# Kernel tuning notes

Measured on AMD Instinct MI355X. Metric: run time of the kernel, lower is better.

## Reference

```python
import jax, jax.numpy as jnp
import numpy as np
import math

ITERATIONS = 2
STRIDE = 1
ALPHA = 0.0
MEAN_DATA = 1.0
FINAL_LAMBDA = 0.01  # final_beta
EPS = 1e-7
MIN_VAR_ADD = 0.0005


def setup_inputs() -> dict:
    key = jax.random.key(0)
    k1, k2 = jax.random.split(key)
    b, h, w, k, i, o, a = 2, 12, 12, 3, 32, 32, 4
    votes = jax.random.normal(k1, (b, h, w, k, k, i, o, a, a), dtype=jnp.float32)
    acts = jax.random.uniform(k2, (b, h, w, k, k, i, 1, 1, 1), dtype=jnp.float32)
    beta_a = jnp.full((1, 1, 1, 1, 1, 1, o, 1, 1), 0.5, dtype=jnp.float32)
    beta_u = jnp.full((1, 1, 1, 1, 1, 1, o, 1, 1), 0.5, dtype=jnp.float32)
    return {"votes": votes, "acts": acts, "beta_a": beta_a, "beta_u": beta_u}


def reference(votes, acts, beta_a, beta_u):
    b, h, w, k = votes.shape[0], votes.shape[1], votes.shape[2], votes.shape[3]
    i, o, a = votes.shape[5], votes.shape[6], votes.shape[7]
    s = STRIDE
    Hr = h * s + k - s  # reconstructed height
    Wr = w * s + k - s
    # target spatial coords for each (h,y) / (w,x) of the kernel window
    Y = jnp.arange(h)[:, None] * s + jnp.arange(k)[None, :]  # (h,k)
    X = jnp.arange(w)[:, None] * s + jnp.arange(k)[None, :]  # (w,k)
    lin = (Y[:, None, :, None] * Wr + X[None, :, None, :]).reshape(-1)  # (h*w*k*k,)

    # R_ij init: softmax over zeros along out-capsule axis -> uniform 1/o
    R = jnp.full((b, h, w, k, k, i, o, 1, 1), 1.0 / o, dtype=votes.dtype)
    out_poses = jnp.zeros((b, h, w, 1, 1, 1, o, a, a), dtype=votes.dtype)

    def m_step(R, out_poses, it):
        Ra = R * acts                                   # (b,h,w,k,k,i,o,1,1)
        sumR = jnp.sum(Ra, axis=(3, 4, 5), keepdims=True)
        mu = jnp.sum(Ra * votes, axis=(3, 4, 5), keepdims=True) / (sumR + EPS)
        mu = (1.0 - ALPHA) * mu + ALPHA * out_poses     # (b,h,w,1,1,1,o,a,a)
        sig = jnp.sum(Ra * jnp.square(votes - mu), axis=(3, 4, 5), keepdims=True) / (sumR + EPS) + MIN_VAR_ADD
        cost = (beta_u - 0.5 * jnp.log(sig + EPS)) * sumR / MEAN_DATA
        inv_temp = FINAL_LAMBDA * (1.0 - 0.95 ** (it + 1))
        a_j = jax.nn.sigmoid(inv_temp * (beta_a - jnp.sum(cost, axis=(-1, -2), keepdims=True)))
        return mu, sig, a_j

    def e_step(mu, sig, a_j):
        log_p = -jnp.sum(jnp.log(2.0 * math.pi * sig) + jnp.square(votes - mu) / (2.0 * sig),
                         axis=(-1, -2), keepdims=True)        # (b,h,w,k,k,i,o,1,1)
        lognum = jnp.log(a_j) + log_p
        ap = jnp.exp(lognum - jnp.max(lognum))                # global-max shift as in original
        # scatter-add (fold / col2im) onto the reconstructed grid, then sum over o
        ap6 = ap.reshape(b, h, w, k, k, i, o)
        ap_t = ap6.transpose(1, 2, 3, 4, 0, 5, 6).reshape(h * w * k * k, b, i, o)
        dense = jax.ops.segment_sum(ap_t, lin, num_segments=Hr * Wr)  # (Hr*Wr,b,i,o)
        dense = dense.sum(-1).reshape(Hr, Wr, b, i)
        # extract_patches: gather the window sums back to (b,h,w,k,k,i)
        denom = dense[Y[:, None, :, None], X[None, :, None, :]]  # (h,w,k,k,b,i)
        denom = jnp.transpose(denom, (4, 0, 1, 2, 3, 5))[..., None, None, None]
        return ap / (denom + EPS)

    for it in range(ITERATIONS - 1):
        mu, sig, a_j = m_step(R, out_poses, it)
        out_poses = mu
        R = e_step(mu, sig, a_j)
    mu, sig, a_j = m_step(R, out_poses, ITERATIONS)

    poses = jnp.squeeze(mu, axis=(3, 4, 5))     # (b,h,w,o,a,a)
    acts_out = jnp.squeeze(a_j, axis=(3, 4, 5))  # (b,h,w,o,1,1)
    return poses, acts_out
```

## Files before the change

### kernel.cpp

```cpp
#include <hip/hip_runtime.h>
#include <math.h>

#define NB 2
#define NH 12
#define NW 12
#define NK 3
#define NI 32
#define NO 32
#define NA 16
#define NBHW (NB*NH*NW)
#define NC (NK*NK*NI)
#define CSTR (NO*NA)
#define VPB (NC*CSTR)
#define HR 14
#define WR 14
#define EPSF 1e-7f
#define MINVAR 5e-4f
#define TEMP0 0.0005f
#define TEMPF 0.00142625f

#define CH 8
#define CPC (NC/CH)
#define ITERS (CPC/2)
#define NBLK (NBHW*CH)

#define PA_S1 0
#define PA_S2 (PA_S1 + NBLK*512)
#define PA_SR (PA_S2 + NBLK*512)
#define PD_S1 (PA_SR + NBLK)
#define PD_S2 (PD_S1 + NBLK*512)
#define PD_SR (PD_S2 + NBLK*512)
#define MU_OFF (PD_SR + NBLK*32)
#define W_OFF  (MU_OFF + NBHW*512)
#define L_OFF  (W_OFF + NBHW*512)
#define BM_OFF (L_OFF + NBHW*32)
#define M_OFF  (BM_OFF + NBLK)
#define DENSE_OFF (M_OFF + 16)
#define DENSE_N (NB*HR*WR*NI)
#define LOGNUM_OFF (DENSE_OFF + DENSE_N)

__global__ __launch_bounds__(256) void kA(const float* __restrict__ votes,
        const float* __restrict__ acts, float* __restrict__ ws) {
    __shared__ float s_acts[CPC];
    __shared__ float4 r1[128], r2[128];
    __shared__ float sR1;
    const int bid = blockIdx.x;
    const int bhw = bid >> 3;
    const int cbase = (bid & 7) * CPC;
    const int t = threadIdx.x;
    if (t < CPC) s_acts[t] = acts[bhw*NC + cbase + t] * (1.0f/NO);
    __syncthreads();
    const int child_sub = t >> 7;
    const int rem = t & 127;
    const float4* vb4 = (const float4*)votes + (size_t)bhw*(VPB/4);
    float s1[4] = {0,0,0,0}, s2[4] = {0,0,0,0};
    float sumR = 0.f;
    #pragma unroll 6
    for (int it = 0; it < ITERS; ++it) {
        const int c_loc = it*2 + child_sub;
        float4 v = vb4[(size_t)(cbase + c_loc)*128 + rem];
        float ra = s_acts[c_loc];
        s1[0] += ra*v.x; s2[0] = fmaf(ra*v.x, v.x, s2[0]);
        s1[1] += ra*v.y; s2[1] = fmaf(ra*v.y, v.y, s2[1]);
        s1[2] += ra*v.z; s2[2] = fmaf(ra*v.z, v.z, s2[2]);
        s1[3] += ra*v.w; s2[3] = fmaf(ra*v.w, v.w, s2[3]);
        sumR += ra;
    }
    if (child_sub) {
        r1[rem] = make_float4(s1[0], s1[1], s1[2], s1[3]);
        r2[rem] = make_float4(s2[0], s2[1], s2[2], s2[3]);
        if (rem == 0) sR1 = sumR;
    }
    __syncthreads();
    if (!child_sub) {
        float4 o1 = r1[rem], o2 = r2[rem];
        ((float4*)(ws + PA_S1))[bid*128 + rem] =
            make_float4(s1[0]+o1.x, s1[1]+o1.y, s1[2]+o1.z, s1[3]+o1.w);
        ((float4*)(ws + PA_S2))[bid*128 + rem] =
            make_float4(s2[0]+o2.x, s2[1]+o2.y, s2[2]+o2.z, s2[3]+o2.w);
        if (rem == 0) ws[PA_SR + bid] = sumR + sR1;
    }
}

__global__ __launch_bounds__(256) void kA2(const float* __restrict__ beta_a,
        const float* __restrict__ beta_u, float* __restrict__ ws) {
    const int bid = blockIdx.x;
    const int bhw = bid >> 1;
    const int obase = (bid & 1) * 16;
    const int t = threadIdx.x;
    const int a = t & 15;
    const int o = obase + (t >> 4);
    const int idx = o*16 + a;
    float s1 = 0.f, s2 = 0.f, sumR = 0.f;
    #pragma unroll
    for (int ch = 0; ch < 8; ++ch) {
        s1   += ws[PA_S1 + (size_t)(bhw*8 + ch)*512 + idx];
        s2   += ws[PA_S2 + (size_t)(bhw*8 + ch)*512 + idx];
        sumR += ws[PA_SR + bhw*8 + ch];
    }
    float mu  = s1 / (sumR + EPSF);
    float sig = (s2 - mu*(2.f*s1 - mu*sumR)) / (sumR + EPSF) + MINVAR;
    ws[MU_OFF + bhw*512 + a*32 + o] = mu;
    ws[W_OFF  + bhw*512 + a*32 + o] = 0.5f / sig;
    float cost = (beta_u[o] - 0.5f*logf(sig + EPSF)) * sumR;
    float ps   = logf(6.2831853071795864f * sig);
    #pragma unroll
    for (int d = 1; d < 16; d <<= 1) {
        cost += __shfl_xor(cost, d);
        ps   += __shfl_xor(ps, d);
    }
    if (a == 0) {
        float aj = 1.0f/(1.0f + expf(-TEMP0*(beta_a[o] - cost)));
        ws[L_OFF + bhw*32 + o] = logf(aj) - ps;
    }
}

__global__ __launch_bounds__(256) void kB(const float* __restrict__ votes,
                                          float* __restrict__ ws) {
    const int bid = blockIdx.x;
    const int bhw = bid >> 3;
    const int cbase = (bid & 7) * CPC;
    const int t = threadIdx.x;
    const int child_sub = t >> 7;
    const int rem = t & 127;
    const int o = rem >> 2;
    const int quad = rem & 3;
    float mur[4], wr[4];
    #pragma unroll
    for (int j = 0; j < 4; ++j) {
        mur[j] = ws[MU_OFF + bhw*512 + (quad*4+j)*32 + o];
        wr[j]  = ws[W_OFF  + bhw*512 + (quad*4+j)*32 + o];
    }
    const float L = ws[L_OFF + bhw*32 + o];
    const float4* vb4 = (const float4*)votes + (size_t)bhw*(VPB/4);
    float* lp = ws + LOGNUM_OFF + (size_t)bhw*(NC*NO);
    float tmax = -3.0e38f;
    #pragma unroll 6
    for (int it = 0; it < ITERS; ++it) {
        const int c = cbase + it*2 + child_sub;
        float4 v = vb4[(size_t)c*128 + rem];
        float d0 = v.x - mur[0];
        float acc = d0*d0*wr[0];
        float d1 = v.y - mur[1]; acc = fmaf(d1*d1, wr[1], acc);
        float d2 = v.z - mur[2]; acc = fmaf(d2*d2, wr[2], acc);
        float d3 = v.w - mur[3]; acc = fmaf(d3*d3, wr[3], acc);
        acc += __shfl_xor(acc, 1);
        acc += __shfl_xor(acc, 2);
        float ln = L - acc;
        if (quad == 0) lp[c*32 + o] = ln;
        tmax = fmaxf(tmax, ln);
    }
    #pragma unroll
    for (int d = 1; d < 64; d <<= 1) tmax = fmaxf(tmax, __shfl_xor(tmax, d));
    __shared__ float smax[4];
    if ((t & 63) == 0) smax[t >> 6] = tmax;
    __syncthreads();
    if (t == 0)
        ws[BM_OFF + bid] = fmaxf(fmaxf(smax[0], smax[1]), fmaxf(smax[2], smax[3]));
}

__global__ __launch_bounds__(256) void kBmax(float* __restrict__ ws) {
    const int t = threadIdx.x;
    float m = -3.0e38f;
    for (int i = t; i < NBLK; i += 256) m = fmaxf(m, ws[BM_OFF + i]);
    #pragma unroll
    for (int d = 1; d < 64; d <<= 1) m = fmaxf(m, __shfl_xor(m, d));
    __shared__ float sm[4];
    if ((t & 63) == 0) sm[t >> 6] = m;
    __syncthreads();
    if (t == 0) ws[M_OFF] = fmaxf(fmaxf(sm[0], sm[1]), fmaxf(sm[2], sm[3]));
}

__global__ __launch_bounds__(256) void kC(float* __restrict__ ws) {
    const int bid = blockIdx.x;
    const int bhw = bid >> 2;
    const int cbase = (bid & 3) * 72;
    const int t = threadIdx.x;
    const int b = bhw / (NH*NW);
    const int rem = bhw % (NH*NW);
    const int y = rem / NW, x = rem % NW;
    const float M = ws[M_OFF];
    const float* lp = ws + LOGNUM_OFF + (size_t)bhw*(NC*NO);
    float* dense = ws + DENSE_OFF;
    const int o = t & 31;
    for (int it = 0; it < 9; ++it) {
        const int c = cbase + it*8 + (t >> 5);
        float s = expf(lp[c*32 + o] - M);
        #pragma unroll
        for (int d = 1; d < 32; d <<= 1) s += __shfl_xor(s, d);
        if (o == 0) {
            const int i = c & 31, kk = c >> 5;
            const int ky = kk / 3, kx = kk % 3;
            atomicAdd(&dense[((b*HR + y+ky)*WR + (x+kx))*NI + i], s);
        }
    }
}

__global__ __launch_bounds__(256) void kD(const float* __restrict__ votes,
        const float* __restrict__ acts, float* __restrict__ ws) {
    __shared__ float s_rd[CPC];
    __shared__ float s_ra[CPC*NO];
    __shared__ float4 r1[128], r2[128];
    __shared__ float sSR[64];
    const int bid = blockIdx.x;
    const int bhw = bid >> 3;
    const int cbase = (bid & 7) * CPC;
    const int t = threadIdx.x;
    const int b = bhw / (NH*NW);
    const int remhw = bhw % (NH*NW);
    const int y = remhw / NW, x = remhw % NW;
    if (t < CPC) {
        const int c = cbase + t;
        const int i = c & 31, kk = c >> 5;
        const int ky = kk / 3, kx = kk % 3;
        float dn = ws[DENSE_OFF + ((b*HR + y+ky)*WR + (x+kx))*NI + i];
        s_rd[t] = acts[bhw*NC + c] / (dn + EPSF);
    }
    __syncthreads();
    const float M = ws[M_OFF];
    const float* lp = ws + LOGNUM_OFF + (size_t)bhw*(NC*NO) + (size_t)cbase*32;
    for (int idx = t; idx < CPC*NO; idx += 256)
        s_ra[idx] = s_rd[idx >> 5] * expf(lp[idx] - M);
    __syncthreads();
    const int child_sub = t >> 7;
    const int rem = t & 127;
    const int o = rem >> 2;
    const int quad = rem & 3;
    const float4* vb4 = (const float4*)votes + (size_t)bhw*(VPB/4);
    float s1[4] = {0,0,0,0}, s2[4] = {0,0,0,0};
    float sumR = 0.f;
    #pragma unroll 6
    for (int it = 0; it < ITERS; ++it) {
        const int c_loc = it*2 + child_sub;
        float4 v = vb4[(size_t)(cbase + c_loc)*128 + rem];
        float ra = s_ra[c_loc*32 + o];
        s1[0] += ra*v.x; s2[0] = fmaf(ra*v.x, v.x, s2[0]);
        s1[1] += ra*v.y; s2[1] = fmaf(ra*v.y, v.y, s2[1]);
        s1[2] += ra*v.z; s2[2] = fmaf(ra*v.z, v.z, s2[2]);
        s1[3] += ra*v.w; s2[3] = fmaf(ra*v.w, v.w, s2[3]);
        sumR += ra;
    }
    if (quad == 0) sSR[child_sub*32 + o] = sumR;
    if (child_sub) {
        r1[rem] = make_float4(s1[0], s1[1], s1[2], s1[3]);
        r2[rem] = make_float4(s2[0], s2[1], s2[2], s2[3]);
    }
    __syncthreads();
    if (!child_sub) {
        float4 o1 = r1[rem], o2 = r2[rem];
        ((float4*)(ws + PD_S1))[bid*128 + rem] =
            make_float4(s1[0]+o1.x, s1[1]+o1.y, s1[2]+o1.z, s1[3]+o1.w);
        ((float4*)(ws + PD_S2))[bid*128 + rem] =
            make_float4(s2[0]+o2.x, s2[1]+o2.y, s2[2]+o2.z, s2[3]+o2.w);
    }
    if (t < 32) ws[PD_SR + bid*32 + t] = sSR[t] + sSR[32 + t];
}

__global__ __launch_bounds__(256) void kD2(const float* __restrict__ beta_a,
        const float* __restrict__ beta_u, const float* __restrict__ ws,
        float* __restrict__ out) {
    const int bid = blockIdx.x;
    const int bhw = bid >> 1;
    const int obase = (bid & 1) * 16;
    const int t = threadIdx.x;
    const int a = t & 15;
    const int o = obase + (t >> 4);
    float s1 = 0.f, s2 = 0.f, sumR = 0.f;
    #pragma unroll
    for (int ch = 0; ch < 8; ++ch) {
        s1   += ws[PD_S1 + (size_t)(bhw*8 + ch)*512 + obase*16 + t];
        s2   += ws[PD_S2 + (size_t)(bhw*8 + ch)*512 + obase*16 + t];
        sumR += ws[PD_SR + (bhw*8 + ch)*32 + o];
    }
    float mu  = s1 / (sumR + EPSF);
    float sig = (s2 - mu*(2.f*s1 - mu*sumR)) / (sumR + EPSF) + MINVAR;
    out[bhw*512 + obase*16 + t] = mu;
    float cost = (beta_u[o] - 0.5f*logf(sig + EPSF)) * sumR;
    #pragma unroll
    for (int d = 1; d < 16; d <<= 1) cost += __shfl_xor(cost, d);
    if (a == 0) {
        float aj = 1.0f/(1.0f + expf(-TEMPF*(beta_a[o] - cost)));
        out[NBHW*512 + bhw*32 + o] = aj;
    }
}

extern "C" void kernel_launch(void* const* d_in, const int* in_sizes, int n_in,
                              void* d_out, int out_size, void* d_ws, size_t ws_size,
                              hipStream_t stream) {
    const float* votes  = (const float*)d_in[0];
    const float* acts   = (const float*)d_in[1];
    const float* beta_a = (const float*)d_in[2];
    const float* beta_u = (const float*)d_in[3];
    float* ws  = (float*)d_ws;
    float* out = (float*)d_out;

    hipMemsetAsync(ws + DENSE_OFF, 0, DENSE_N*sizeof(float), stream);
    kA   <<<NBLK,   256, 0, stream>>>(votes, acts, ws);
    kA2  <<<NBHW*2, 256, 0, stream>>>(beta_a, beta_u, ws);
    kB   <<<NBLK,   256, 0, stream>>>(votes, ws);
    kBmax<<<1,      256, 0, stream>>>(ws);
    kC   <<<NBHW*4, 256, 0, stream>>>(ws);
    kD   <<<NBLK,   256, 0, stream>>>(votes, acts, ws);
    kD2  <<<NBHW*2, 256, 0, stream>>>(beta_a, beta_u, ws, out);
}
```

Measured before the change: 317.3 us.

## Fuse reduction kernels into neighbors, drop memset, and halve chunk split

Removes the memset, kA2 and kBmax launches. Dense zeroing now happens inside kA. The per-bhw mu/sigma/L finalisation is computed redundantly in each kB block into shared memory. Each block of kC and kD recomputes the global max from the per-block maxima. Chunks per bhw drop from 8 to 4, which halves the block count but doubles the per-block loop length. This cuts launch overhead and intermediate global round-trips, at the cost of redundant finalisation work and lower parallelism over the 1.3 MB-per-bhw vote stream.

```diff
diff --git a/kernel.cpp b/kernel.cpp
--- a/kernel.cpp
+++ b/kernel.cpp
@@ -19,7 +19,7 @@
 #define TEMP0 0.0005f
 #define TEMPF 0.00142625f
 
-#define CH 8
+#define CH 4
 #define CPC (NC/CH)
 #define ITERS (CPC/2)
 #define NBLK (NBHW*CH)
@@ -30,12 +30,8 @@
 #define PD_S1 (PA_SR + NBLK)
 #define PD_S2 (PD_S1 + NBLK*512)
 #define PD_SR (PD_S2 + NBLK*512)
-#define MU_OFF (PD_SR + NBLK*32)
-#define W_OFF  (MU_OFF + NBHW*512)
-#define L_OFF  (W_OFF + NBHW*512)
-#define BM_OFF (L_OFF + NBHW*32)
-#define M_OFF  (BM_OFF + NBLK)
-#define DENSE_OFF (M_OFF + 16)
+#define BM_OFF (PD_SR + NBLK*32)
+#define DENSE_OFF (BM_OFF + NBLK)
 #define DENSE_N (NB*HR*WR*NI)
 #define LOGNUM_OFF (DENSE_OFF + DENSE_N)
 
@@ -45,9 +41,13 @@
     __shared__ float4 r1[128], r2[128];
     __shared__ float sR1;
     const int bid = blockIdx.x;
-    const int bhw = bid >> 3;
-    const int cbase = (bid & 7) * CPC;
-    const int t = threadIdx.x;
+    const int bhw = bid >> 2;
+    const int cbase = (bid & 3) * CPC;
+    const int t = threadIdx.x;
+    {
+        const int idx = bid*256 + t;
+        if (idx < DENSE_N) ws[DENSE_OFF + idx] = 0.f;
+    }
     if (t < CPC) s_acts[t] = acts[bhw*NC + cbase + t] * (1.0f/NO);
     __syncthreads();
     const int child_sub = t >> 7;
@@ -82,45 +82,44 @@
     }
 }
 
-__global__ __launch_bounds__(256) void kA2(const float* __restrict__ beta_a,
-        const float* __restrict__ beta_u, float* __restrict__ ws) {
-    const int bid = blockIdx.x;
-    const int bhw = bid >> 1;
-    const int obase = (bid & 1) * 16;
-    const int t = threadIdx.x;
-    const int a = t & 15;
-    const int o = obase + (t >> 4);
-    const int idx = o*16 + a;
-    float s1 = 0.f, s2 = 0.f, sumR = 0.f;
-    #pragma unroll
-    for (int ch = 0; ch < 8; ++ch) {
-        s1   += ws[PA_S1 + (size_t)(bhw*8 + ch)*512 + idx];
-        s2   += ws[PA_S2 + (size_t)(bhw*8 + ch)*512 + idx];
-        sumR += ws[PA_SR + bhw*8 + ch];
-    }
-    float mu  = s1 / (sumR + EPSF);
-    float sig = (s2 - mu*(2.f*s1 - mu*sumR)) / (sumR + EPSF) + MINVAR;
-    ws[MU_OFF + bhw*512 + a*32 + o] = mu;
-    ws[W_OFF  + bhw*512 + a*32 + o] = 0.5f / sig;
-    float cost = (beta_u[o] - 0.5f*logf(sig + EPSF)) * sumR;
-    float ps   = logf(6.2831853071795864f * sig);
-    #pragma unroll
-    for (int d = 1; d < 16; d <<= 1) {
-        cost += __shfl_xor(cost, d);
-        ps   += __shfl_xor(ps, d);
-    }
-    if (a == 0) {
-        float aj = 1.0f/(1.0f + expf(-TEMP0*(beta_a[o] - cost)));
-        ws[L_OFF + bhw*32 + o] = logf(aj) - ps;
-    }
-}
-
 __global__ __launch_bounds__(256) void kB(const float* __restrict__ votes,
-                                          float* __restrict__ ws) {
-    const int bid = blockIdx.x;
-    const int bhw = bid >> 3;
-    const int cbase = (bid & 7) * CPC;
-    const int t = threadIdx.x;
+        const float* __restrict__ beta_a, const float* __restrict__ beta_u,
+        float* __restrict__ ws) {
+    __shared__ float s_mu[512], s_w[512], s_L[32], smax[4];
+    const int bid = blockIdx.x;
+    const int bhw = bid >> 2;
+    const int cbase = (bid & 3) * CPC;
+    const int t = threadIdx.x;
+    float sumR = 0.f;
+    #pragma unroll
+    for (int ch = 0; ch < CH; ++ch) sumR += ws[PA_SR + bhw*CH + ch];
+    #pragma unroll
+    for (int half = 0; half < 2; ++half) {
+        const int idx = t + half*256;
+        float s1 = 0.f, s2 = 0.f;
+        #pragma unroll
+        for (int ch = 0; ch < CH; ++ch) {
+            s1 += ws[PA_S1 + (size_t)(bhw*CH + ch)*512 + idx];
+            s2 += ws[PA_S2 + (size_t)(bhw*CH + ch)*512 + idx];
+        }
+        const int o = idx >> 4, a = idx & 15;
+        float mu  = s1 / (sumR + EPSF);
+        float sig = (s2 - mu*(2.f*s1 - mu*sumR)) / (sumR + EPSF) + MINVAR;
+        s_mu[a*32 + o] = mu;
+        s_w [a*32 + o] = 0.5f / sig;
+        float cost = (beta_u[o] - 0.5f*logf(sig + EPSF)) * sumR;
+        float ps   = logf(6.2831853071795864f * sig);
+        #pragma unroll
+        for (int d = 1; d < 16; d <<= 1) {
+            cost += __shfl_xor(cost, d);
+            ps   += __shfl_xor(ps, d);
+        }
+        if (a == 0) {
+            float aj = 1.0f/(1.0f + expf(-TEMP0*(beta_a[o] - cost)));
+            s_L[o] = logf(aj) - ps;
+        }
+    }
+    __syncthreads();
     const int child_sub = t >> 7;
     const int rem = t & 127;
     const int o = rem >> 2;
@@ -128,10 +127,10 @@
     float mur[4], wr[4];
     #pragma unroll
     for (int j = 0; j < 4; ++j) {
-        mur[j] = ws[MU_OFF + bhw*512 + (quad*4+j)*32 + o];
-        wr[j]  = ws[W_OFF  + bhw*512 + (quad*4+j)*32 + o];
-    }
-    const float L = ws[L_OFF + bhw*32 + o];
+        mur[j] = s_mu[(quad*4 + j)*32 + o];
+        wr[j]  = s_w [(quad*4 + j)*32 + o];
+    }
+    const float L = s_L[o];
     const float4* vb4 = (const float4*)votes + (size_t)bhw*(VPB/4);
     float* lp = ws + LOGNUM_OFF + (size_t)bhw*(NC*NO);
     float tmax = -3.0e38f;
@@ -152,38 +151,32 @@
     }
     #pragma unroll
     for (int d = 1; d < 64; d <<= 1) tmax = fmaxf(tmax, __shfl_xor(tmax, d));
-    __shared__ float smax[4];
     if ((t & 63) == 0) smax[t >> 6] = tmax;
     __syncthreads();
     if (t == 0)
         ws[BM_OFF + bid] = fmaxf(fmaxf(smax[0], smax[1]), fmaxf(smax[2], smax[3]));
 }
 
-__global__ __launch_bounds__(256) void kBmax(float* __restrict__ ws) {
+__global__ __launch_bounds__(256) void kC(float* __restrict__ ws) {
+    __shared__ float smax[4];
+    const int bid = blockIdx.x;
+    const int bhw = bid >> 2;
+    const int cbase = (bid & 3) * CPC;
     const int t = threadIdx.x;
     float m = -3.0e38f;
     for (int i = t; i < NBLK; i += 256) m = fmaxf(m, ws[BM_OFF + i]);
     #pragma unroll
     for (int d = 1; d < 64; d <<= 1) m = fmaxf(m, __shfl_xor(m, d));
-    __shared__ float sm[4];
-    if ((t & 63) == 0) sm[t >> 6] = m;
-    __syncthreads();
-    if (t == 0) ws[M_OFF] = fmaxf(fmaxf(sm[0], sm[1]), fmaxf(sm[2], sm[3]));
-}
-
-__global__ __launch_bounds__(256) void kC(float* __restrict__ ws) {
-    const int bid = blockIdx.x;
-    const int bhw = bid >> 2;
-    const int cbase = (bid & 3) * 72;
-    const int t = threadIdx.x;
+    if ((t & 63) == 0) smax[t >> 6] = m;
+    __syncthreads();
+    const float M = fmaxf(fmaxf(smax[0], smax[1]), fmaxf(smax[2], smax[3]));
     const int b = bhw / (NH*NW);
     const int rem = bhw % (NH*NW);
     const int y = rem / NW, x = rem % NW;
-    const float M = ws[M_OFF];
     const float* lp = ws + LOGNUM_OFF + (size_t)bhw*(NC*NO);
     float* dense = ws + DENSE_OFF;
     const int o = t & 31;
-    for (int it = 0; it < 9; ++it) {
+    for (int it = 0; it < CPC/8; ++it) {
         const int c = cbase + it*8 + (t >> 5);
         float s = expf(lp[c*32 + o] - M);
         #pragma unroll
@@ -200,15 +193,21 @@
         const float* __restrict__ acts, float* __restrict__ ws) {
     __shared__ float s_rd[CPC];
     __shared__ float s_ra[CPC*NO];
+    __shared__ float smax[4];
     __shared__ float4 r1[128], r2[128];
     __shared__ float sSR[64];
     const int bid = blockIdx.x;
-    const int bhw = bid >> 3;
-    const int cbase = (bid & 7) * CPC;
+    const int bhw = bid >> 2;
+    const int cbase = (bid & 3) * CPC;
     const int t = threadIdx.x;
     const int b = bhw / (NH*NW);
     const int remhw = bhw % (NH*NW);
     const int y = remhw / NW, x = remhw % NW;
+    float m = -3.0e38f;
+    for (int i = t; i < NBLK; i += 256) m = fmaxf(m, ws[BM_OFF + i]);
+    #pragma unroll
+    for (int d = 1; d < 64; d <<= 1) m = fmaxf(m, __shfl_xor(m, d));
+    if ((t & 63) == 0) smax[t >> 6] = m;
     if (t < CPC) {
         const int c = cbase + t;
         const int i = c & 31, kk = c >> 5;
@@ -217,7 +216,7 @@
         s_rd[t] = acts[bhw*NC + c] / (dn + EPSF);
     }
     __syncthreads();
-    const float M = ws[M_OFF];
+    const float M = fmaxf(fmaxf(smax[0], smax[1]), fmaxf(smax[2], smax[3]));
     const float* lp = ws + LOGNUM_OFF + (size_t)bhw*(NC*NO) + (size_t)cbase*32;
     for (int idx = t; idx < CPC*NO; idx += 256)
         s_ra[idx] = s_rd[idx >> 5] * expf(lp[idx] - M);
@@ -267,10 +266,10 @@
     const int o = obase + (t >> 4);
     float s1 = 0.f, s2 = 0.f, sumR = 0.f;
     #pragma unroll
-    for (int ch = 0; ch < 8; ++ch) {
-        s1   += ws[PD_S1 + (size_t)(bhw*8 + ch)*512 + obase*16 + t];
-        s2   += ws[PD_S2 + (size_t)(bhw*8 + ch)*512 + obase*16 + t];
-        sumR += ws[PD_SR + (bhw*8 + ch)*32 + o];
+    for (int ch = 0; ch < CH; ++ch) {
+        s1   += ws[PD_S1 + (size_t)(bhw*CH + ch)*512 + obase*16 + t];
+        s2   += ws[PD_S2 + (size_t)(bhw*CH + ch)*512 + obase*16 + t];
+        sumR += ws[PD_SR + (bhw*CH + ch)*32 + o];
     }
     float mu  = s1 / (sumR + EPSF);
     float sig = (s2 - mu*(2.f*s1 - mu*sumR)) / (sumR + EPSF) + MINVAR;
@@ -294,12 +293,9 @@
     float* ws  = (float*)d_ws;
     float* out = (float*)d_out;
 
-    hipMemsetAsync(ws + DENSE_OFF, 0, DENSE_N*sizeof(float), stream);
-    kA   <<<NBLK,   256, 0, stream>>>(votes, acts, ws);
-    kA2  <<<NBHW*2, 256, 0, stream>>>(beta_a, beta_u, ws);
-    kB   <<<NBLK,   256, 0, stream>>>(votes, ws);
-    kBmax<<<1,      256, 0, stream>>>(ws);
-    kC   <<<NBHW*4, 256, 0, stream>>>(ws);
-    kD   <<<NBLK,   256, 0, stream>>>(votes, acts, ws);
-    kD2  <<<NBHW*2, 256, 0, stream>>>(beta_a, beta_u, ws, out);
-}
+    kA <<<NBLK,   256, 0, stream>>>(votes, acts, ws);
+    kB <<<NBLK,   256, 0, stream>>>(votes, beta_a, beta_u, ws);
+    kC <<<NBHW*4, 256, 0, stream>>>(ws);
+    kD <<<NBLK,   256, 0, stream>>>(votes, acts, ws);
+    kD2<<<NBHW*2, 256, 0, stream>>>(beta_a, beta_u, ws, out);
+}
```

After: 308.7 us. 2.7% less time.
